# Performance work log

Hardware: AMD Instinct MI355X
Metric: run time of the kernel (lower is better)

The kernel has to match this reference:

```python
import jax, jax.numpy as jnp
import numpy as np

N_NODES = 100000
N_EDGES = 1600000
D = 32
N_GRAPHS = 128


def setup_inputs() -> dict:
    key = jax.random.key(0)
    ks = jax.random.split(key, 6)
    feats = jax.random.normal(ks[0], (N_NODES, D), dtype=jnp.float32)
    src = jax.random.randint(ks[1], (N_EDGES,), 0, N_NODES, dtype=jnp.int32)
    dst = jax.random.randint(ks[2], (N_EDGES,), 0, N_NODES, dtype=jnp.int32)
    graph_ids = jnp.sort(jax.random.randint(ks[3], (N_NODES,), 0, N_GRAPHS, dtype=jnp.int32))
    # Linear weights (torch nn.Linear: y = x @ W.T + b); store as [in, out] here
    W1 = jax.random.normal(ks[4], (D, D), dtype=jnp.float32) * (1.0 / np.sqrt(D))
    b1 = jnp.zeros((D,), dtype=jnp.float32)
    W2 = jax.random.normal(ks[5], (D, D), dtype=jnp.float32) * (1.0 / np.sqrt(D))
    b2 = jnp.zeros((D,), dtype=jnp.float32)
    return {"feats": feats, "src": src, "dst": dst, "graph_ids": graph_ids,
            "W1": W1, "b1": b1, "W2": W2, "b2": b2}


def _gin_conv(x, src, dst, W, b):
    # DGL GINConv, aggregator 'sum', eps=0 (default, non-learnable):
    # h_v = Linear(x_v + sum_{u in N(v)} x_u)
    agg = jax.ops.segment_sum(x[src], dst, num_segments=N_NODES)
    return (x + agg) @ W + b


def reference(feats, src, dst, graph_ids, W1, b1, W2, b2):
    h = _gin_conv(feats, src, dst, W1, b1)          # conv1
    h = jax.nn.relu(h)                               # F.relu
    h = _gin_conv(h, src, dst, W2, b2)               # conv2
    # SumPooling: sum node features per graph -> [N_GRAPHS, D]
    return jax.ops.segment_sum(h, graph_ids, num_segments=N_GRAPHS)
```

## Files before the change

### kernel.cpp

```cpp
#include <hip/hip_runtime.h>
#include <hip/hip_bf16.h>

#define N_NODES 100000
#define N_EDGES 1600000
#define D 32
#define N_GRAPHS 128

#define WIN 128
#define NWINS ((N_NODES + WIN - 1) / WIN)
#define CAP 2560
#define NODES_PER_WAVE 8

__global__ void bin_kernel(const int* __restrict__ src,
                           const int* __restrict__ dst,
                           int* __restrict__ gfill,
                           int* __restrict__ ebuf) {
    __shared__ int lhist[NWINS];
    __shared__ int lbase[NWINS];
    const int tid = threadIdx.x;
    const int per = (N_EDGES + gridDim.x - 1) / gridDim.x;
    const int e0 = blockIdx.x * per;
    const int e1 = (e0 + per < N_EDGES) ? e0 + per : N_EDGES;

    for (int b = tid; b < NWINS; b += blockDim.x) lhist[b] = 0;
    __syncthreads();
    for (int e = e0 + tid; e < e1; e += blockDim.x)
        atomicAdd(&lhist[dst[e] >> 7], 1);
    __syncthreads();
    for (int b = tid; b < NWINS; b += blockDim.x) {
        int c = lhist[b];
        lbase[b] = c ? atomicAdd(&gfill[b], c) : 0;
        lhist[b] = 0;
    }
    __syncthreads();
    for (int e = e0 + tid; e < e1; e += blockDim.x) {
        int d = dst[e];
        int bn = d >> 7;
        int r = atomicAdd(&lhist[bn], 1);
        int off = lbase[bn] + r;
        if (off < CAP) ebuf[bn * CAP + off] = ((d & (WIN - 1)) << 17) | src[e];
    }
}

__global__ void wscan_kernel(const int* __restrict__ gfill, int* __restrict__ wbase) {
    __shared__ int s[1024];
    const int t = threadIdx.x;
    int v = (t < NWINS) ? gfill[t] : 0;
    s[t] = v;
    __syncthreads();
    for (int off = 1; off < 1024; off <<= 1) {
        int a = (t >= off) ? s[t - off] : 0;
        __syncthreads();
        s[t] += a;
        __syncthreads();
    }
    if (t < NWINS) wbase[t] = s[t] - v;
    if (t == NWINS - 1) wbase[NWINS] = s[t];
}

__global__ void csr_local_kernel(const int* __restrict__ ebuf,
                                 const int* __restrict__ wbase,
                                 int* __restrict__ esrc,
                                 int* __restrict__ rend,
                                 int* __restrict__ deg) {
    __shared__ int pk[CAP];
    __shared__ int ssrc[CAP];
    __shared__ int hs[WIN];
    __shared__ int hcnt[WIN];
    __shared__ int cur[WIN];
    const int tid = threadIdx.x;
    const int w = blockIdx.x;
    const int base_out = wbase[w];
    int cnt = wbase[w + 1] - base_out;
    if (cnt > CAP) cnt = CAP;
    const int n0 = w * WIN;

    for (int i = tid; i < cnt; i += 256) pk[i] = ebuf[w * CAP + i];
    if (tid < WIN) hcnt[tid] = 0;
    __syncthreads();
    for (int i = tid; i < cnt; i += 256) atomicAdd(&hcnt[pk[i] >> 17], 1);
    __syncthreads();
    if (tid < WIN) hs[tid] = hcnt[tid];
    __syncthreads();
    for (int off = 1; off < WIN; off <<= 1) {
        int a = 0;
        if (tid < WIN && tid >= off) a = hs[tid - off];
        __syncthreads();
        if (tid < WIN) hs[tid] += a;
        __syncthreads();
    }
    if (tid < WIN) {
        const int incl = hs[tid];
        const int c = hcnt[tid];
        cur[tid] = incl - c;
        const int n = n0 + tid;
        if (n < N_NODES) { rend[n] = base_out + incl; deg[n] = c; }
    }
    __syncthreads();
    for (int i = tid; i < cnt; i += 256) {
        const int p = pk[i];
        const int pos = atomicAdd(&cur[p >> 17], 1);
        ssrc[pos] = p & 0x1FFFF;
    }
    __syncthreads();
    for (int i = tid; i < cnt; i += 256) esrc[base_out + i] = ssrc[i];
}

template <bool RELU, bool POOL>
__global__ void gin_layer_kernel(const float* __restrict__ x,
                                 const int* __restrict__ esrc,
                                 const int* __restrict__ rend,
                                 const int* __restrict__ deg,
                                 const float* __restrict__ W,
                                 const float* __restrict__ b,
                                 const int* __restrict__ graph_ids,
                                 float* __restrict__ out) {
    const int lane = threadIdx.x & 63;
    const int es = lane >> 3;
    const int fq = lane & 7;

    float w[4][4];
#pragma unroll
    for (int k = 0; k < 4; ++k) {
        const float4 wv = *reinterpret_cast<const float4*>(&W[(es * 4 + k) * D + fq * 4]);
        w[k][0] = wv.x; w[k][1] = wv.y; w[k][2] = wv.z; w[k][3] = wv.w;
    }
    const float4 bv = *reinterpret_cast<const float4*>(&b[fq * 4]);

    const int wid = blockIdx.x * (blockDim.x >> 6) + (threadIdx.x >> 6);
    const int v0 = wid * NODES_PER_WAVE;
    if (v0 >= N_NODES) return;
    const int v1 = (v0 + NODES_PER_WAVE < N_NODES) ? v0 + NODES_PER_WAVE : N_NODES;

    float p0 = 0.f, p1 = 0.f, p2 = 0.f, p3 = 0.f;
    int cur_g = POOL ? graph_ids[v0] : 0;

    for (int v = v0; v < v1; ++v) {
        const int end = rend[v];
        const int dg = deg[v];
        int e = end - dg;

        float a0, a1, a2, a3;
        if (es == 0) {
            const float4 xv = *reinterpret_cast<const float4*>(&x[(size_t)v * D + fq * 4]);
            a0 = xv.x; a1 = xv.y; a2 = xv.z; a3 = xv.w;
        } else { a0 = a1 = a2 = a3 = 0.f; }

        for (; e + 16 <= end; e += 16) {
            const int s0 = esrc[e + es];
            const int s1 = esrc[e + 8 + es];
            const float4 g0 = *reinterpret_cast<const float4*>(&x[(size_t)s0 * D + fq * 4]);
            const float4 g1 = *reinterpret_cast<const float4*>(&x[(size_t)s1 * D + fq * 4]);
            a0 += g0.x; a1 += g0.y; a2 += g0.z; a3 += g0.w;
            a0 += g1.x; a1 += g1.y; a2 += g1.z; a3 += g1.w;
        }
        if (e + 8 <= end) {
            const int s0 = esrc[e + es];
            const float4 g0 = *reinterpret_cast<const float4*>(&x[(size_t)s0 * D + fq * 4]);
            a0 += g0.x; a1 += g0.y; a2 += g0.z; a3 += g0.w;
            e += 8;
        }
        const int rem = end - e;
        if (es < rem) {
            const int s0 = esrc[e + es];
            const float4 g0 = *reinterpret_cast<const float4*>(&x[(size_t)s0 * D + fq * 4]);
            a0 += g0.x; a1 += g0.y; a2 += g0.z; a3 += g0.w;
        }

        a0 += __shfl_xor(a0, 8);  a1 += __shfl_xor(a1, 8);  a2 += __shfl_xor(a2, 8);  a3 += __shfl_xor(a3, 8);
        a0 += __shfl_xor(a0, 16); a1 += __shfl_xor(a1, 16); a2 += __shfl_xor(a2, 16); a3 += __shfl_xor(a3, 16);
        a0 += __shfl_xor(a0, 32); a1 += __shfl_xor(a1, 32); a2 += __shfl_xor(a2, 32); a3 += __shfl_xor(a3, 32);

        const float q0 = __shfl(a0, es, 8);
        const float q1 = __shfl(a1, es, 8);
        const float q2 = __shfl(a2, es, 8);
        const float q3 = __shfl(a3, es, 8);

        float y0 = q0 * w[0][0] + q1 * w[1][0] + q2 * w[2][0] + q3 * w[3][0];
        float y1 = q0 * w[0][1] + q1 * w[1][1] + q2 * w[2][1] + q3 * w[3][1];
        float y2 = q0 * w[0][2] + q1 * w[1][2] + q2 * w[2][2] + q3 * w[3][2];
        float y3 = q0 * w[0][3] + q1 * w[1][3] + q2 * w[2][3] + q3 * w[3][3];

        y0 += __shfl_xor(y0, 8);  y1 += __shfl_xor(y1, 8);  y2 += __shfl_xor(y2, 8);  y3 += __shfl_xor(y3, 8);
        y0 += __shfl_xor(y0, 16); y1 += __shfl_xor(y1, 16); y2 += __shfl_xor(y2, 16); y3 += __shfl_xor(y3, 16);
        y0 += __shfl_xor(y0, 32); y1 += __shfl_xor(y1, 32); y2 += __shfl_xor(y2, 32); y3 += __shfl_xor(y3, 32);

        y0 += bv.x; y1 += bv.y; y2 += bv.z; y3 += bv.w;
        if (RELU) {
            y0 = fmaxf(y0, 0.f); y1 = fmaxf(y1, 0.f); y2 = fmaxf(y2, 0.f); y3 = fmaxf(y3, 0.f);
        }

        if (POOL) {
            const int g = graph_ids[v];
            if (g != cur_g) {
                if (es == 0) {
                    atomicAdd(&out[cur_g * D + fq * 4 + 0], p0);
                    atomicAdd(&out[cur_g * D + fq * 4 + 1], p1);
                    atomicAdd(&out[cur_g * D + fq * 4 + 2], p2);
                    atomicAdd(&out[cur_g * D + fq * 4 + 3], p3);
                }
                p0 = p1 = p2 = p3 = 0.f;
                cur_g = g;
            }
            p0 += y0; p1 += y1; p2 += y2; p3 += y3;
        } else {
            if (es == 0) {
                float4 o; o.x = y0; o.y = y1; o.z = y2; o.w = y3;
                *reinterpret_cast<float4*>(&out[(size_t)v * D + fq * 4]) = o;
            }
        }
    }
    if (POOL && es == 0) {
        atomicAdd(&out[cur_g * D + fq * 4 + 0], p0);
        atomicAdd(&out[cur_g * D + fq * 4 + 1], p1);
        atomicAdd(&out[cur_g * D + fq * 4 + 2], p2);
        atomicAdd(&out[cur_g * D + fq * 4 + 3], p3);
    }
}

extern "C" void kernel_launch(void* const* d_in, const int* in_sizes, int n_in,
                              void* d_out, int out_size, void* d_ws, size_t ws_size,
                              hipStream_t stream) {
    const float* feats = (const float*)d_in[0];
    const int* src = (const int*)d_in[1];
    const int* dst = (const int*)d_in[2];
    const int* graph_ids = (const int*)d_in[3];
    const float* W1 = (const float*)d_in[4];
    const float* b1 = (const float*)d_in[5];
    const float* W2 = (const float*)d_in[6];
    const float* b2 = (const float*)d_in[7];
    float* out = (float*)d_out;

    int* gfill = (int*)d_ws;
    int* wbase = gfill + 1024;
    int* ebuf  = wbase + 1024;
    int* esrc  = ebuf + (size_t)NWINS * CAP;
    int* rend  = esrc + N_EDGES;
    int* deg   = rend + N_NODES;
    float* h   = (float*)(deg + N_NODES);

    const int total_waves = (N_NODES + NODES_PER_WAVE - 1) / NODES_PER_WAVE;
    const int layer_blocks = (total_waves + 3) / 4;

    hipMemsetAsync(gfill, 0, 1024 * sizeof(int), stream);
    bin_kernel<<<256, 512, 0, stream>>>(src, dst, gfill, ebuf);
    wscan_kernel<<<1, 1024, 0, stream>>>(gfill, wbase);
    csr_local_kernel<<<NWINS, 256, 0, stream>>>(ebuf, wbase, esrc, rend, deg);

    gin_layer_kernel<true, false><<<layer_blocks, 256, 0, stream>>>(
        feats, esrc, rend, deg, W1, b1, graph_ids, h);

    hipMemsetAsync(out, 0, (size_t)out_size * sizeof(float), stream);
    gin_layer_kernel<false, true><<<layer_blocks, 256, 0, stream>>>(
        h, esrc, rend, deg, W2, b2, graph_ids, out);
}
```

Measured before the change: 144.4 us.

## Store node features in bf16 and gather 16 edges per wave iteration

Adds a pass that converts the input features to packed bf16, and has layer 1 write its hidden output in bf16. Both GIN layers now gather bf16 rows, so each neighbour row costs 64 bytes instead of 128, and 16 edges are processed per step instead of 8. Accumulation, the matmul and pooling stay in fp32. This cuts the bytes moved by the random-access gather but loses precision in the stored features and adds one extra conversion kernel.

```diff
diff --git a/kernel.cpp b/kernel.cpp
--- a/kernel.cpp
+++ b/kernel.cpp
@@ -106,26 +106,52 @@
     for (int i = tid; i < cnt; i += 256) esrc[base_out + i] = ssrc[i];
 }
 
+__device__ __forceinline__ unsigned pk2bf(float a, float b) {
+    unsigned ua = __float_as_uint(a); ua = (ua + 0x7fffu + ((ua >> 16) & 1u)) >> 16;
+    unsigned ub = __float_as_uint(b); ub = (ub + 0x7fffu + ((ub >> 16) & 1u)) >> 16;
+    return ua | (ub << 16);
+}
+
+__global__ void f32_to_bf16_kernel(const float* __restrict__ in, uint4* __restrict__ out) {
+    const int i = blockIdx.x * blockDim.x + threadIdx.x;
+    if (i >= N_NODES * D / 8) return;
+    const float4* p = reinterpret_cast<const float4*>(in) + (size_t)i * 2;
+    const float4 v0 = p[0], v1 = p[1];
+    uint4 o;
+    o.x = pk2bf(v0.x, v0.y); o.y = pk2bf(v0.z, v0.w);
+    o.z = pk2bf(v1.x, v1.y); o.w = pk2bf(v1.z, v1.w);
+    out[i] = o;
+}
+
+#define CVT_ADD(g) do { \
+    acc0 += __uint_as_float((g).x << 16); acc1 += __uint_as_float((g).x & 0xffff0000u); \
+    acc2 += __uint_as_float((g).y << 16); acc3 += __uint_as_float((g).y & 0xffff0000u); \
+    acc4 += __uint_as_float((g).z << 16); acc5 += __uint_as_float((g).z & 0xffff0000u); \
+    acc6 += __uint_as_float((g).w << 16); acc7 += __uint_as_float((g).w & 0xffff0000u); } while (0)
+
 template <bool RELU, bool POOL>
-__global__ void gin_layer_kernel(const float* __restrict__ x,
+__global__ void gin_layer_kernel(const uint4* __restrict__ xbf,
                                  const int* __restrict__ esrc,
                                  const int* __restrict__ rend,
                                  const int* __restrict__ deg,
                                  const float* __restrict__ W,
-                                 const float* __restrict__ b,
+                                 const float* __restrict__ bias,
                                  const int* __restrict__ graph_ids,
-                                 float* __restrict__ out) {
+                                 float* __restrict__ outf,
+                                 uint2* __restrict__ outbf) {
     const int lane = threadIdx.x & 63;
-    const int es = lane >> 3;
-    const int fq = lane & 7;
+    const int fq = lane & 3;
+    const int es = lane >> 2;
+    const int og = lane & 7;
+    const int ig = lane >> 3;
 
     float w[4][4];
 #pragma unroll
     for (int k = 0; k < 4; ++k) {
-        const float4 wv = *reinterpret_cast<const float4*>(&W[(es * 4 + k) * D + fq * 4]);
-        w[k][0] = wv.x; w[k][1] = wv.y; w[k][2] = wv.z; w[k][3] = wv.w;
-    }
-    const float4 bv = *reinterpret_cast<const float4*>(&b[fq * 4]);
+        const float4 t = *reinterpret_cast<const float4*>(&W[(ig * 4 + k) * D + og * 4]);
+        w[k][0] = t.x; w[k][1] = t.y; w[k][2] = t.z; w[k][3] = t.w;
+    }
+    const float4 bv = *reinterpret_cast<const float4*>(&bias[og * 4]);
 
     const int wid = blockIdx.x * (blockDim.x >> 6) + (threadIdx.x >> 6);
     const int v0 = wid * NODES_PER_WAVE;
@@ -137,54 +163,59 @@
 
     for (int v = v0; v < v1; ++v) {
         const int end = rend[v];
-        const int dg = deg[v];
-        int e = end - dg;
-
-        float a0, a1, a2, a3;
+        int e = end - deg[v];
+
+        float acc0 = 0.f, acc1 = 0.f, acc2 = 0.f, acc3 = 0.f;
+        float acc4 = 0.f, acc5 = 0.f, acc6 = 0.f, acc7 = 0.f;
         if (es == 0) {
-            const float4 xv = *reinterpret_cast<const float4*>(&x[(size_t)v * D + fq * 4]);
-            a0 = xv.x; a1 = xv.y; a2 = xv.z; a3 = xv.w;
-        } else { a0 = a1 = a2 = a3 = 0.f; }
-
-        for (; e + 16 <= end; e += 16) {
-            const int s0 = esrc[e + es];
-            const int s1 = esrc[e + 8 + es];
-            const float4 g0 = *reinterpret_cast<const float4*>(&x[(size_t)s0 * D + fq * 4]);
-            const float4 g1 = *reinterpret_cast<const float4*>(&x[(size_t)s1 * D + fq * 4]);
-            a0 += g0.x; a1 += g0.y; a2 += g0.z; a3 += g0.w;
-            a0 += g1.x; a1 += g1.y; a2 += g1.z; a3 += g1.w;
-        }
-        if (e + 8 <= end) {
-            const int s0 = esrc[e + es];
-            const float4 g0 = *reinterpret_cast<const float4*>(&x[(size_t)s0 * D + fq * 4]);
-            a0 += g0.x; a1 += g0.y; a2 += g0.z; a3 += g0.w;
-            e += 8;
+            const uint4 sv = xbf[(size_t)v * 4 + fq];
+            CVT_ADD(sv);
+        }
+
+        for (; e + 32 <= end; e += 32) {
+            const int r0 = esrc[e + es] & 0x1FFFF;
+            const int r1 = esrc[e + 16 + es] & 0x1FFFF;
+            const uint4 g0 = xbf[(size_t)r0 * 4 + fq];
+            const uint4 g1 = xbf[(size_t)r1 * 4 + fq];
+            CVT_ADD(g0); CVT_ADD(g1);
+        }
+        if (e + 16 <= end) {
+            const int r0 = esrc[e + es] & 0x1FFFF;
+            const uint4 g0 = xbf[(size_t)r0 * 4 + fq];
+            CVT_ADD(g0);
+            e += 16;
         }
         const int rem = end - e;
         if (es < rem) {
-            const int s0 = esrc[e + es];
-            const float4 g0 = *reinterpret_cast<const float4*>(&x[(size_t)s0 * D + fq * 4]);
-            a0 += g0.x; a1 += g0.y; a2 += g0.z; a3 += g0.w;
-        }
-
-        a0 += __shfl_xor(a0, 8);  a1 += __shfl_xor(a1, 8);  a2 += __shfl_xor(a2, 8);  a3 += __shfl_xor(a3, 8);
-        a0 += __shfl_xor(a0, 16); a1 += __shfl_xor(a1, 16); a2 += __shfl_xor(a2, 16); a3 += __shfl_xor(a3, 16);
-        a0 += __shfl_xor(a0, 32); a1 += __shfl_xor(a1, 32); a2 += __shfl_xor(a2, 32); a3 += __shfl_xor(a3, 32);
-
-        const float q0 = __shfl(a0, es, 8);
-        const float q1 = __shfl(a1, es, 8);
-        const float q2 = __shfl(a2, es, 8);
-        const float q3 = __shfl(a3, es, 8);
+            const int r0 = esrc[e + es] & 0x1FFFF;
+            const uint4 g0 = xbf[(size_t)r0 * 4 + fq];
+            CVT_ADD(g0);
+        }
+
+#pragma unroll
+        for (int off = 4; off <= 32; off <<= 1) {
+            acc0 += __shfl_xor(acc0, off); acc1 += __shfl_xor(acc1, off);
+            acc2 += __shfl_xor(acc2, off); acc3 += __shfl_xor(acc3, off);
+            acc4 += __shfl_xor(acc4, off); acc5 += __shfl_xor(acc5, off);
+            acc6 += __shfl_xor(acc6, off); acc7 += __shfl_xor(acc7, off);
+        }
+
+        const int s = ig >> 1;
+        const int hi = ig & 1;
+        const float l0 = __shfl(acc0, s), l1 = __shfl(acc1, s), l2 = __shfl(acc2, s), l3 = __shfl(acc3, s);
+        const float h0 = __shfl(acc4, s), h1 = __shfl(acc5, s), h2 = __shfl(acc6, s), h3 = __shfl(acc7, s);
+        const float q0 = hi ? h0 : l0, q1 = hi ? h1 : l1, q2 = hi ? h2 : l2, q3 = hi ? h3 : l3;
 
         float y0 = q0 * w[0][0] + q1 * w[1][0] + q2 * w[2][0] + q3 * w[3][0];
         float y1 = q0 * w[0][1] + q1 * w[1][1] + q2 * w[2][1] + q3 * w[3][1];
         float y2 = q0 * w[0][2] + q1 * w[1][2] + q2 * w[2][2] + q3 * w[3][2];
         float y3 = q0 * w[0][3] + q1 * w[1][3] + q2 * w[2][3] + q3 * w[3][3];
 
-        y0 += __shfl_xor(y0, 8);  y1 += __shfl_xor(y1, 8);  y2 += __shfl_xor(y2, 8);  y3 += __shfl_xor(y3, 8);
-        y0 += __shfl_xor(y0, 16); y1 += __shfl_xor(y1, 16); y2 += __shfl_xor(y2, 16); y3 += __shfl_xor(y3, 16);
-        y0 += __shfl_xor(y0, 32); y1 += __shfl_xor(y1, 32); y2 += __shfl_xor(y2, 32); y3 += __shfl_xor(y3, 32);
-
+#pragma unroll
+        for (int off = 8; off <= 32; off <<= 1) {
+            y0 += __shfl_xor(y0, off); y1 += __shfl_xor(y1, off);
+            y2 += __shfl_xor(y2, off); y3 += __shfl_xor(y3, off);
+        }
         y0 += bv.x; y1 += bv.y; y2 += bv.z; y3 += bv.w;
         if (RELU) {
             y0 = fmaxf(y0, 0.f); y1 = fmaxf(y1, 0.f); y2 = fmaxf(y2, 0.f); y3 = fmaxf(y3, 0.f);
@@ -193,28 +224,26 @@
         if (POOL) {
             const int g = graph_ids[v];
             if (g != cur_g) {
-                if (es == 0) {
-                    atomicAdd(&out[cur_g * D + fq * 4 + 0], p0);
-                    atomicAdd(&out[cur_g * D + fq * 4 + 1], p1);
-                    atomicAdd(&out[cur_g * D + fq * 4 + 2], p2);
-                    atomicAdd(&out[cur_g * D + fq * 4 + 3], p3);
+                if (ig == 0) {
+                    atomicAdd(&outf[cur_g * D + og * 4 + 0], p0);
+                    atomicAdd(&outf[cur_g * D + og * 4 + 1], p1);
+                    atomicAdd(&outf[cur_g * D + og * 4 + 2], p2);
+                    atomicAdd(&outf[cur_g * D + og * 4 + 3], p3);
                 }
                 p0 = p1 = p2 = p3 = 0.f;
                 cur_g = g;
             }
             p0 += y0; p1 += y1; p2 += y2; p3 += y3;
-        } else {
-            if (es == 0) {
-                float4 o; o.x = y0; o.y = y1; o.z = y2; o.w = y3;
-                *reinterpret_cast<float4*>(&out[(size_t)v * D + fq * 4]) = o;
-            }
-        }
-    }
-    if (POOL && es == 0) {
-        atomicAdd(&out[cur_g * D + fq * 4 + 0], p0);
-        atomicAdd(&out[cur_g * D + fq * 4 + 1], p1);
-        atomicAdd(&out[cur_g * D + fq * 4 + 2], p2);
-        atomicAdd(&out[cur_g * D + fq * 4 + 3], p3);
+        } else if (ig == 0) {
+            uint2 o; o.x = pk2bf(y0, y1); o.y = pk2bf(y2, y3);
+            outbf[(size_t)v * 8 + og] = o;
+        }
+    }
+    if (POOL && ig == 0) {
+        atomicAdd(&outf[cur_g * D + og * 4 + 0], p0);
+        atomicAdd(&outf[cur_g * D + og * 4 + 1], p1);
+        atomicAdd(&outf[cur_g * D + og * 4 + 2], p2);
+        atomicAdd(&outf[cur_g * D + og * 4 + 3], p3);
     }
 }
 
@@ -237,7 +266,8 @@
     int* esrc  = ebuf + (size_t)NWINS * CAP;
     int* rend  = esrc + N_EDGES;
     int* deg   = rend + N_NODES;
-    float* h   = (float*)(deg + N_NODES);
+    unsigned* xbf = (unsigned*)(deg + N_NODES);
+    unsigned* hbf = xbf + (size_t)N_NODES * (D / 2);
 
     const int total_waves = (N_NODES + NODES_PER_WAVE - 1) / NODES_PER_WAVE;
     const int layer_blocks = (total_waves + 3) / 4;
@@ -247,10 +277,13 @@
     wscan_kernel<<<1, 1024, 0, stream>>>(gfill, wbase);
     csr_local_kernel<<<NWINS, 256, 0, stream>>>(ebuf, wbase, esrc, rend, deg);
 
+    f32_to_bf16_kernel<<<(N_NODES * D / 8 + 255) / 256, 256, 0, stream>>>(
+        feats, (uint4*)xbf);
+
     gin_layer_kernel<true, false><<<layer_blocks, 256, 0, stream>>>(
-        feats, esrc, rend, deg, W1, b1, graph_ids, h);
+        (const uint4*)xbf, esrc, rend, deg, W1, b1, graph_ids, nullptr, (uint2*)hbf);
 
     hipMemsetAsync(out, 0, (size_t)out_size * sizeof(float), stream);
     gin_layer_kernel<false, true><<<layer_blocks, 256, 0, stream>>>(
-        h, esrc, rend, deg, W2, b2, graph_ids, out);
-}
+        (const uint4*)hbf, esrc, rend, deg, W2, b2, graph_ids, out, nullptr);
+}
```

Result: slower. 185.6 us (+28.5%).

## Process two nodes per wave with half-wave gathers and LDS-staged edge indices

Applied to the files above, without the earlier changes.

Each wave now handles two nodes at once, one per half-wave, instead of eight nodes one after another. The wave loads its contiguous CSR edge indices into shared memory up front. Aggregated rows are staged through shared memory so the 32x32 linear step reads them directly instead of going through cross-lane shuffle broadcasts. This trades a serial per-node loop for more waves and more parallel memory gathers, at the cost of block-level syncs, divergence from the two nodes' differing degrees, and a global fallback for index spans past 128.

```diff
diff --git a/kernel.cpp b/kernel.cpp
--- a/kernel.cpp
+++ b/kernel.cpp
@@ -9,7 +9,8 @@
 #define WIN 128
 #define NWINS ((N_NODES + WIN - 1) / WIN)
 #define CAP 2560
-#define NODES_PER_WAVE 8
+#define NPW 2
+#define IDXCAP 128
 
 __global__ void bin_kernel(const int* __restrict__ src,
                            const int* __restrict__ dst,
@@ -107,114 +108,137 @@
 }
 
 template <bool RELU, bool POOL>
-__global__ void gin_layer_kernel(const float* __restrict__ x,
-                                 const int* __restrict__ esrc,
-                                 const int* __restrict__ rend,
-                                 const int* __restrict__ deg,
-                                 const float* __restrict__ W,
-                                 const float* __restrict__ b,
-                                 const int* __restrict__ graph_ids,
-                                 float* __restrict__ out) {
+__global__ void __launch_bounds__(256)
+gin_layer_kernel(const float* __restrict__ x,
+                 const int* __restrict__ esrc,
+                 const int* __restrict__ rend,
+                 const int* __restrict__ deg,
+                 const float* __restrict__ W,
+                 const float* __restrict__ bias,
+                 const int* __restrict__ graph_ids,
+                 float* __restrict__ out) {
+    __shared__ int   lidx[4][IDXCAP];
+    __shared__ float lagg[4][NPW * D];
     const int lane = threadIdx.x & 63;
-    const int es = lane >> 3;
+    const int wslot = threadIdx.x >> 6;
+    const int g  = lane >> 5;
+    const int es = (lane >> 3) & 3;
     const int fq = lane & 7;
 
+    const int og = lane & 7;
+    const int ig = lane >> 3;
     float w[4][4];
 #pragma unroll
     for (int k = 0; k < 4; ++k) {
-        const float4 wv = *reinterpret_cast<const float4*>(&W[(es * 4 + k) * D + fq * 4]);
-        w[k][0] = wv.x; w[k][1] = wv.y; w[k][2] = wv.z; w[k][3] = wv.w;
-    }
-    const float4 bv = *reinterpret_cast<const float4*>(&b[fq * 4]);
-
-    const int wid = blockIdx.x * (blockDim.x >> 6) + (threadIdx.x >> 6);
-    const int v0 = wid * NODES_PER_WAVE;
-    if (v0 >= N_NODES) return;
-    const int v1 = (v0 + NODES_PER_WAVE < N_NODES) ? v0 + NODES_PER_WAVE : N_NODES;
-
-    float p0 = 0.f, p1 = 0.f, p2 = 0.f, p3 = 0.f;
+        const float4 t = *reinterpret_cast<const float4*>(&W[(ig * 4 + k) * D + og * 4]);
+        w[k][0] = t.x; w[k][1] = t.y; w[k][2] = t.z; w[k][3] = t.w;
+    }
+    const float4 bv = *reinterpret_cast<const float4*>(&bias[og * 4]);
+
+    const int wid = blockIdx.x * 4 + wslot;
+    const int v0 = wid * NPW;
+    const int vg = v0 + g;
+    const int dg = deg[vg];
+    const int sg = rend[vg] - dg;
+    const int S = __shfl(sg, 0);
+    const int offg = sg - S;
+
+    int t0 = S + lane;      if (t0 > N_EDGES - 1) t0 = N_EDGES - 1;
+    int t1 = S + 64 + lane; if (t1 > N_EDGES - 1) t1 = N_EDGES - 1;
+    lidx[wslot][lane] = esrc[t0];
+    lidx[wslot][64 + lane] = esrc[t1];
+    __syncthreads();
+
+    int Jn = (dg + 3) >> 2;
+    int Jmax = Jn;
+    { int t = __shfl_xor(Jmax, 32); Jmax = Jmax > t ? Jmax : t; }
+
+    float a0 = 0.f, a1 = 0.f, a2 = 0.f, a3 = 0.f;
+    if (es == 0) {
+        const float4 sv = *reinterpret_cast<const float4*>(&x[(size_t)vg * D + fq * 4]);
+        a0 = sv.x; a1 = sv.y; a2 = sv.z; a3 = sv.w;
+    }
+
+    for (int c = 0; c < Jmax; c += 4) {
+        const int e0 = (c + 0) * 4 + es; const bool b0 = e0 < dg; const int o0 = offg + e0;
+        const int e1 = (c + 1) * 4 + es; const bool b1 = e1 < dg; const int o1 = offg + e1;
+        const int e2 = (c + 2) * 4 + es; const bool b2 = e2 < dg; const int o2 = offg + e2;
+        const int e3 = (c + 3) * 4 + es; const bool b3 = e3 < dg; const int o3 = offg + e3;
+
+        int p0 = lidx[wslot][o0 < IDXCAP ? o0 : 0];
+        int p1 = lidx[wslot][o1 < IDXCAP ? o1 : 0];
+        int p2 = lidx[wslot][o2 < IDXCAP ? o2 : 0];
+        int p3 = lidx[wslot][o3 < IDXCAP ? o3 : 0];
+        if (b0 && o0 >= IDXCAP) p0 = esrc[S + o0];
+        if (b1 && o1 >= IDXCAP) p1 = esrc[S + o1];
+        if (b2 && o2 >= IDXCAP) p2 = esrc[S + o2];
+        if (b3 && o3 >= IDXCAP) p3 = esrc[S + o3];
+
+        if (b0) { const float4 G = *reinterpret_cast<const float4*>(&x[(size_t)p0 * D + fq * 4]);
+                  a0 += G.x; a1 += G.y; a2 += G.z; a3 += G.w; }
+        if (b1) { const float4 G = *reinterpret_cast<const float4*>(&x[(size_t)p1 * D + fq * 4]);
+                  a0 += G.x; a1 += G.y; a2 += G.z; a3 += G.w; }
+        if (b2) { const float4 G = *reinterpret_cast<const float4*>(&x[(size_t)p2 * D + fq * 4]);
+                  a0 += G.x; a1 += G.y; a2 += G.z; a3 += G.w; }
+        if (b3) { const float4 G = *reinterpret_cast<const float4*>(&x[(size_t)p3 * D + fq * 4]);
+                  a0 += G.x; a1 += G.y; a2 += G.z; a3 += G.w; }
+    }
+
+    a0 += __shfl_xor(a0, 8);  a1 += __shfl_xor(a1, 8);
+    a2 += __shfl_xor(a2, 8);  a3 += __shfl_xor(a3, 8);
+    a0 += __shfl_xor(a0, 16); a1 += __shfl_xor(a1, 16);
+    a2 += __shfl_xor(a2, 16); a3 += __shfl_xor(a3, 16);
+
+    if (es == 0) {
+        float4 o; o.x = a0; o.y = a1; o.z = a2; o.w = a3;
+        *reinterpret_cast<float4*>(&lagg[wslot][g * D + fq * 4]) = o;
+    }
+    __syncthreads();
+
+    float pl0 = 0.f, pl1 = 0.f, pl2 = 0.f, pl3 = 0.f;
     int cur_g = POOL ? graph_ids[v0] : 0;
-
-    for (int v = v0; v < v1; ++v) {
-        const int end = rend[v];
-        const int dg = deg[v];
-        int e = end - dg;
-
-        float a0, a1, a2, a3;
-        if (es == 0) {
-            const float4 xv = *reinterpret_cast<const float4*>(&x[(size_t)v * D + fq * 4]);
-            a0 = xv.x; a1 = xv.y; a2 = xv.z; a3 = xv.w;
-        } else { a0 = a1 = a2 = a3 = 0.f; }
-
-        for (; e + 16 <= end; e += 16) {
-            const int s0 = esrc[e + es];
-            const int s1 = esrc[e + 8 + es];
-            const float4 g0 = *reinterpret_cast<const float4*>(&x[(size_t)s0 * D + fq * 4]);
-            const float4 g1 = *reinterpret_cast<const float4*>(&x[(size_t)s1 * D + fq * 4]);
-            a0 += g0.x; a1 += g0.y; a2 += g0.z; a3 += g0.w;
-            a0 += g1.x; a1 += g1.y; a2 += g1.z; a3 += g1.w;
-        }
-        if (e + 8 <= end) {
-            const int s0 = esrc[e + es];
-            const float4 g0 = *reinterpret_cast<const float4*>(&x[(size_t)s0 * D + fq * 4]);
-            a0 += g0.x; a1 += g0.y; a2 += g0.z; a3 += g0.w;
-            e += 8;
-        }
-        const int rem = end - e;
-        if (es < rem) {
-            const int s0 = esrc[e + es];
-            const float4 g0 = *reinterpret_cast<const float4*>(&x[(size_t)s0 * D + fq * 4]);
-            a0 += g0.x; a1 += g0.y; a2 += g0.z; a3 += g0.w;
-        }
-
-        a0 += __shfl_xor(a0, 8);  a1 += __shfl_xor(a1, 8);  a2 += __shfl_xor(a2, 8);  a3 += __shfl_xor(a3, 8);
-        a0 += __shfl_xor(a0, 16); a1 += __shfl_xor(a1, 16); a2 += __shfl_xor(a2, 16); a3 += __shfl_xor(a3, 16);
-        a0 += __shfl_xor(a0, 32); a1 += __shfl_xor(a1, 32); a2 += __shfl_xor(a2, 32); a3 += __shfl_xor(a3, 32);
-
-        const float q0 = __shfl(a0, es, 8);
-        const float q1 = __shfl(a1, es, 8);
-        const float q2 = __shfl(a2, es, 8);
-        const float q3 = __shfl(a3, es, 8);
-
-        float y0 = q0 * w[0][0] + q1 * w[1][0] + q2 * w[2][0] + q3 * w[3][0];
-        float y1 = q0 * w[0][1] + q1 * w[1][1] + q2 * w[2][1] + q3 * w[3][1];
-        float y2 = q0 * w[0][2] + q1 * w[1][2] + q2 * w[2][2] + q3 * w[3][2];
-        float y3 = q0 * w[0][3] + q1 * w[1][3] + q2 * w[2][3] + q3 * w[3][3];
-
-        y0 += __shfl_xor(y0, 8);  y1 += __shfl_xor(y1, 8);  y2 += __shfl_xor(y2, 8);  y3 += __shfl_xor(y3, 8);
-        y0 += __shfl_xor(y0, 16); y1 += __shfl_xor(y1, 16); y2 += __shfl_xor(y2, 16); y3 += __shfl_xor(y3, 16);
-        y0 += __shfl_xor(y0, 32); y1 += __shfl_xor(y1, 32); y2 += __shfl_xor(y2, 32); y3 += __shfl_xor(y3, 32);
-
+#pragma unroll
+    for (int n = 0; n < NPW; ++n) {
+        const int v = v0 + n;
+        const float4 q = *reinterpret_cast<const float4*>(&lagg[wslot][n * D + ig * 4]);
+        float y0 = q.x * w[0][0] + q.y * w[1][0] + q.z * w[2][0] + q.w * w[3][0];
+        float y1 = q.x * w[0][1] + q.y * w[1][1] + q.z * w[2][1] + q.w * w[3][1];
+        float y2 = q.x * w[0][2] + q.y * w[1][2] + q.z * w[2][2] + q.w * w[3][2];
+        float y3 = q.x * w[0][3] + q.y * w[1][3] + q.z * w[2][3] + q.w * w[3][3];
+        y0 += __shfl_xor(y0, 8);  y1 += __shfl_xor(y1, 8);
+        y2 += __shfl_xor(y2, 8);  y3 += __shfl_xor(y3, 8);
+        y0 += __shfl_xor(y0, 16); y1 += __shfl_xor(y1, 16);
+        y2 += __shfl_xor(y2, 16); y3 += __shfl_xor(y3, 16);
+        y0 += __shfl_xor(y0, 32); y1 += __shfl_xor(y1, 32);
+        y2 += __shfl_xor(y2, 32); y3 += __shfl_xor(y3, 32);
         y0 += bv.x; y1 += bv.y; y2 += bv.z; y3 += bv.w;
         if (RELU) {
-            y0 = fmaxf(y0, 0.f); y1 = fmaxf(y1, 0.f); y2 = fmaxf(y2, 0.f); y3 = fmaxf(y3, 0.f);
+            y0 = fmaxf(y0, 0.f); y1 = fmaxf(y1, 0.f);
+            y2 = fmaxf(y2, 0.f); y3 = fmaxf(y3, 0.f);
         }
-
         if (POOL) {
-            const int g = graph_ids[v];
-            if (g != cur_g) {
-                if (es == 0) {
-                    atomicAdd(&out[cur_g * D + fq * 4 + 0], p0);
-                    atomicAdd(&out[cur_g * D + fq * 4 + 1], p1);
-                    atomicAdd(&out[cur_g * D + fq * 4 + 2], p2);
-                    atomicAdd(&out[cur_g * D + fq * 4 + 3], p3);
+            const int gg = graph_ids[v];
+            if (gg != cur_g) {
+                if (ig == 0) {
+                    atomicAdd(&out[cur_g * D + og * 4 + 0], pl0);
+                    atomicAdd(&out[cur_g * D + og * 4 + 1], pl1);
+                    atomicAdd(&out[cur_g * D + og * 4 + 2], pl2);
+                    atomicAdd(&out[cur_g * D + og * 4 + 3], pl3);
                 }
-                p0 = p1 = p2 = p3 = 0.f;
-                cur_g = g;
+                pl0 = pl1 = pl2 = pl3 = 0.f;
+                cur_g = gg;
             }
-            p0 += y0; p1 += y1; p2 += y2; p3 += y3;
-        } else {
-            if (es == 0) {
-                float4 o; o.x = y0; o.y = y1; o.z = y2; o.w = y3;
-                *reinterpret_cast<float4*>(&out[(size_t)v * D + fq * 4]) = o;
-            }
+            pl0 += y0; pl1 += y1; pl2 += y2; pl3 += y3;
+        } else if (ig == 0) {
+            float4 o; o.x = y0; o.y = y1; o.z = y2; o.w = y3;
+            *reinterpret_cast<float4*>(&out[(size_t)v * D + og * 4]) = o;
         }
     }
-    if (POOL && es == 0) {
-        atomicAdd(&out[cur_g * D + fq * 4 + 0], p0);
-        atomicAdd(&out[cur_g * D + fq * 4 + 1], p1);
-        atomicAdd(&out[cur_g * D + fq * 4 + 2], p2);
-        atomicAdd(&out[cur_g * D + fq * 4 + 3], p3);
+    if (POOL && ig == 0) {
+        atomicAdd(&out[cur_g * D + og * 4 + 0], pl0);
+        atomicAdd(&out[cur_g * D + og * 4 + 1], pl1);
+        atomicAdd(&out[cur_g * D + og * 4 + 2], pl2);
+        atomicAdd(&out[cur_g * D + og * 4 + 3], pl3);
     }
 }
 
@@ -239,7 +263,7 @@
     int* deg   = rend + N_NODES;
     float* h   = (float*)(deg + N_NODES);
 
-    const int total_waves = (N_NODES + NODES_PER_WAVE - 1) / NODES_PER_WAVE;
+    const int total_waves = (N_NODES + NPW - 1) / NPW;
     const int layer_blocks = (total_waves + 3) / 4;
 
     hipMemsetAsync(gfill, 0, 1024 * sizeof(int), stream);
```

Result: slower. 232.8 us (+61.2%).

## Batch edge-index and gather loads across all eight nodes per wave

Applied to the files above, without the earlier changes.

Restructures the GIN layer kernel so each wave first loads degree, row end and graph id for its eight nodes in one lane-parallel read. It then issues the first sixteen edge-index and feature-gather loads for all eight nodes together before reducing. The aim is more memory-level parallelism and less serial latency per node. Bounds checks are dropped because the code assumes N_NODES divides evenly by 32, and the per-node accumulators raise register pressure.

```diff
diff --git a/kernel.cpp b/kernel.cpp
--- a/kernel.cpp
+++ b/kernel.cpp
@@ -9,7 +9,7 @@
 #define WIN 128
 #define NWINS ((N_NODES + WIN - 1) / WIN)
 #define CAP 2560
-#define NODES_PER_WAVE 8
+#define NPW 8
 
 __global__ void bin_kernel(const int* __restrict__ src,
                            const int* __restrict__ dst,
@@ -107,14 +107,15 @@
 }
 
 template <bool RELU, bool POOL>
-__global__ void gin_layer_kernel(const float* __restrict__ x,
-                                 const int* __restrict__ esrc,
-                                 const int* __restrict__ rend,
-                                 const int* __restrict__ deg,
-                                 const float* __restrict__ W,
-                                 const float* __restrict__ b,
-                                 const int* __restrict__ graph_ids,
-                                 float* __restrict__ out) {
+__global__ void __launch_bounds__(256)
+gin_layer_kernel(const float* __restrict__ x,
+                 const int* __restrict__ esrc,
+                 const int* __restrict__ rend,
+                 const int* __restrict__ deg,
+                 const float* __restrict__ W,
+                 const float* __restrict__ bias,
+                 const int* __restrict__ graph_ids,
+                 float* __restrict__ out) {
     const int lane = threadIdx.x & 63;
     const int es = lane >> 3;
     const int fq = lane & 7;
@@ -122,51 +123,72 @@
     float w[4][4];
 #pragma unroll
     for (int k = 0; k < 4; ++k) {
-        const float4 wv = *reinterpret_cast<const float4*>(&W[(es * 4 + k) * D + fq * 4]);
-        w[k][0] = wv.x; w[k][1] = wv.y; w[k][2] = wv.z; w[k][3] = wv.w;
-    }
-    const float4 bv = *reinterpret_cast<const float4*>(&b[fq * 4]);
-
-    const int wid = blockIdx.x * (blockDim.x >> 6) + (threadIdx.x >> 6);
-    const int v0 = wid * NODES_PER_WAVE;
-    if (v0 >= N_NODES) return;
-    const int v1 = (v0 + NODES_PER_WAVE < N_NODES) ? v0 + NODES_PER_WAVE : N_NODES;
-
-    float p0 = 0.f, p1 = 0.f, p2 = 0.f, p3 = 0.f;
-    int cur_g = POOL ? graph_ids[v0] : 0;
-
-    for (int v = v0; v < v1; ++v) {
-        const int end = rend[v];
-        const int dg = deg[v];
-        int e = end - dg;
-
-        float a0, a1, a2, a3;
-        if (es == 0) {
-            const float4 xv = *reinterpret_cast<const float4*>(&x[(size_t)v * D + fq * 4]);
-            a0 = xv.x; a1 = xv.y; a2 = xv.z; a3 = xv.w;
-        } else { a0 = a1 = a2 = a3 = 0.f; }
-
-        for (; e + 16 <= end; e += 16) {
-            const int s0 = esrc[e + es];
-            const int s1 = esrc[e + 8 + es];
-            const float4 g0 = *reinterpret_cast<const float4*>(&x[(size_t)s0 * D + fq * 4]);
-            const float4 g1 = *reinterpret_cast<const float4*>(&x[(size_t)s1 * D + fq * 4]);
-            a0 += g0.x; a1 += g0.y; a2 += g0.z; a3 += g0.w;
-            a0 += g1.x; a1 += g1.y; a2 += g1.z; a3 += g1.w;
-        }
-        if (e + 8 <= end) {
-            const int s0 = esrc[e + es];
-            const float4 g0 = *reinterpret_cast<const float4*>(&x[(size_t)s0 * D + fq * 4]);
-            a0 += g0.x; a1 += g0.y; a2 += g0.z; a3 += g0.w;
-            e += 8;
-        }
-        const int rem = end - e;
-        if (es < rem) {
-            const int s0 = esrc[e + es];
-            const float4 g0 = *reinterpret_cast<const float4*>(&x[(size_t)s0 * D + fq * 4]);
-            a0 += g0.x; a1 += g0.y; a2 += g0.z; a3 += g0.w;
-        }
-
+        const float4 t = *reinterpret_cast<const float4*>(&W[(es * 4 + k) * D + fq * 4]);
+        w[k][0] = t.x; w[k][1] = t.y; w[k][2] = t.z; w[k][3] = t.w;
+    }
+    const float4 bv = *reinterpret_cast<const float4*>(&bias[fq * 4]);
+
+    const int wid = blockIdx.x * 4 + (threadIdx.x >> 6);
+    const int v0 = wid * NPW;
+
+    const int vv = v0 + (lane & 7);
+    const int rend_v = rend[vv];
+    const int deg_v = deg[vv];
+    const int gid_v = POOL ? graph_ids[vv] : 0;
+
+    const float4 sv = *reinterpret_cast<const float4*>(&x[(size_t)(v0 + es) * D + fq * 4]);
+
+    float acc[8][4];
+#pragma unroll
+    for (int n = 0; n < 8; ++n) { acc[n][0] = 0.f; acc[n][1] = 0.f; acc[n][2] = 0.f; acc[n][3] = 0.f; }
+#pragma unroll
+    for (int n = 0; n < 8; ++n) {
+        if (es == n) { acc[n][0] += sv.x; acc[n][1] += sv.y; acc[n][2] += sv.z; acc[n][3] += sv.w; }
+    }
+
+    int Dn[8], Sn[8];
+#pragma unroll
+    for (int n = 0; n < 8; ++n) {
+        Dn[n] = __shfl(deg_v, n);
+        Sn[n] = __shfl(rend_v, n) - Dn[n];
+    }
+
+    int idx0[8], idx1[8];
+#pragma unroll
+    for (int n = 0; n < 8; ++n) {
+        idx0[n] = (es < Dn[n]) ? esrc[Sn[n] + es] : -1;
+        idx1[n] = (8 + es < Dn[n]) ? esrc[Sn[n] + 8 + es] : -1;
+    }
+#pragma unroll
+    for (int n = 0; n < 8; ++n) {
+        if (idx0[n] >= 0) {
+            const float4 G = *reinterpret_cast<const float4*>(&x[(size_t)idx0[n] * D + fq * 4]);
+            acc[n][0] += G.x; acc[n][1] += G.y; acc[n][2] += G.z; acc[n][3] += G.w;
+        }
+        if (idx1[n] >= 0) {
+            const float4 G = *reinterpret_cast<const float4*>(&x[(size_t)idx1[n] * D + fq * 4]);
+            acc[n][0] += G.x; acc[n][1] += G.y; acc[n][2] += G.z; acc[n][3] += G.w;
+        }
+    }
+
+#pragma unroll
+    for (int n = 0; n < 8; ++n) {
+        const int Rn = Sn[n] + Dn[n];
+        for (int e = Sn[n] + 16; e < Rn; e += 8) {
+            const int r = e + es;
+            if (r < Rn) {
+                const int s0 = esrc[r];
+                const float4 G = *reinterpret_cast<const float4*>(&x[(size_t)s0 * D + fq * 4]);
+                acc[n][0] += G.x; acc[n][1] += G.y; acc[n][2] += G.z; acc[n][3] += G.w;
+            }
+        }
+    }
+
+    float pl0 = 0.f, pl1 = 0.f, pl2 = 0.f, pl3 = 0.f;
+    int cur_g = POOL ? __shfl(gid_v, 0) : 0;
+#pragma unroll
+    for (int n = 0; n < 8; ++n) {
+        float a0 = acc[n][0], a1 = acc[n][1], a2 = acc[n][2], a3 = acc[n][3];
         a0 += __shfl_xor(a0, 8);  a1 += __shfl_xor(a1, 8);  a2 += __shfl_xor(a2, 8);  a3 += __shfl_xor(a3, 8);
         a0 += __shfl_xor(a0, 16); a1 += __shfl_xor(a1, 16); a2 += __shfl_xor(a2, 16); a3 += __shfl_xor(a3, 16);
         a0 += __shfl_xor(a0, 32); a1 += __shfl_xor(a1, 32); a2 += __shfl_xor(a2, 32); a3 += __shfl_xor(a3, 32);
@@ -191,30 +213,28 @@
         }
 
         if (POOL) {
-            const int g = graph_ids[v];
-            if (g != cur_g) {
+            const int gg = __shfl(gid_v, n);
+            if (gg != cur_g) {
                 if (es == 0) {
-                    atomicAdd(&out[cur_g * D + fq * 4 + 0], p0);
-                    atomicAdd(&out[cur_g * D + fq * 4 + 1], p1);
-                    atomicAdd(&out[cur_g * D + fq * 4 + 2], p2);
-                    atomicAdd(&out[cur_g * D + fq * 4 + 3], p3);
+                    atomicAdd(&out[cur_g * D + fq * 4 + 0], pl0);
+                    atomicAdd(&out[cur_g * D + fq * 4 + 1], pl1);
+                    atomicAdd(&out[cur_g * D + fq * 4 + 2], pl2);
+                    atomicAdd(&out[cur_g * D + fq * 4 + 3], pl3);
                 }
-                p0 = p1 = p2 = p3 = 0.f;
-                cur_g = g;
+                pl0 = pl1 = pl2 = pl3 = 0.f;
+                cur_g = gg;
             }
-            p0 += y0; p1 += y1; p2 += y2; p3 += y3;
-        } else {
-            if (es == 0) {
-                float4 o; o.x = y0; o.y = y1; o.z = y2; o.w = y3;
-                *reinterpret_cast<float4*>(&out[(size_t)v * D + fq * 4]) = o;
-            }
+            pl0 += y0; pl1 += y1; pl2 += y2; pl3 += y3;
+        } else if (es == 0) {
+            float4 o; o.x = y0; o.y = y1; o.z = y2; o.w = y3;
+            *reinterpret_cast<float4*>(&out[(size_t)(v0 + n) * D + fq * 4]) = o;
         }
     }
     if (POOL && es == 0) {
-        atomicAdd(&out[cur_g * D + fq * 4 + 0], p0);
-        atomicAdd(&out[cur_g * D + fq * 4 + 1], p1);
-        atomicAdd(&out[cur_g * D + fq * 4 + 2], p2);
-        atomicAdd(&out[cur_g * D + fq * 4 + 3], p3);
+        atomicAdd(&out[cur_g * D + fq * 4 + 0], pl0);
+        atomicAdd(&out[cur_g * D + fq * 4 + 1], pl1);
+        atomicAdd(&out[cur_g * D + fq * 4 + 2], pl2);
+        atomicAdd(&out[cur_g * D + fq * 4 + 3], pl3);
     }
 }
 
@@ -239,8 +259,8 @@
     int* deg   = rend + N_NODES;
     float* h   = (float*)(deg + N_NODES);
 
-    const int total_waves = (N_NODES + NODES_PER_WAVE - 1) / NODES_PER_WAVE;
-    const int layer_blocks = (total_waves + 3) / 4;
+    const int total_waves = N_NODES / NPW;
+    const int layer_blocks = total_waves / 4;
 
     hipMemsetAsync(gfill, 0, 1024 * sizeof(int), stream);
     bin_kernel<<<256, 512, 0, stream>>>(src, dst, gfill, ebuf);
```

Measured after the change: 200.1 us. +38.6%, slower.
